# Optimization experiments

Hardware: AMD Instinct MI355X
Metric: run time of the kernel (lower is better)

## Reference

```python
import jax, jax.numpy as jnp
import numpy as np

NUM_POINTS = 4_000_000
RADIUS = 2.5
IMG = 1024


def setup_inputs() -> dict:
    key = jax.random.key(0)
    k1, k2, k3, k4 = jax.random.split(key, 4)
    # Uniform sampling inside a sphere, mirroring the torch __init__
    phi = jax.random.uniform(k1, (NUM_POINTS,)) * 2 * np.pi
    costheta = jax.random.uniform(k2, (NUM_POINTS,)) * 2 - 1
    u = jax.random.uniform(k3, (NUM_POINTS,))
    theta = jnp.arccos(costheta)
    r = RADIUS * u ** (1.0 / 3.0)
    x = r * jnp.sin(theta) * jnp.cos(phi)
    y = r * jnp.sin(theta) * jnp.sin(phi)
    z = r * jnp.cos(theta)
    positions = jnp.stack([x, y, z], axis=-1).astype(jnp.float32)  # [N,3]
    colors = jax.random.uniform(k4, (NUM_POINTS, 3), dtype=jnp.float32)
    # Camera at origin looking down +z, points translated to z in [2.5, 7.5]
    camera_pose = jnp.eye(4, dtype=jnp.float32).at[2, 3].set(5.0)
    intrinsics = jnp.array([[800.0, 0.0, 512.0],
                            [0.0, 800.0, 512.0],
                            [0.0, 0.0, 1.0]], dtype=jnp.float32)
    return {"positions": positions, "colors": colors,
            "camera_pose": camera_pose, "intrinsics": intrinsics,
            "H": IMG, "W": IMG}


def reference(positions, colors, camera_pose, intrinsics, H, W):
    # points_cam = (R @ P^T)^T + t^T
    R = camera_pose[:3, :3]
    t = camera_pose[:3, 3]
    pc = positions @ R.T + t  # [N,3]
    x, y, z = pc[:, 0], pc[:, 1], pc[:, 2]
    fx, fy = intrinsics[0, 0], intrinsics[1, 1]
    cx, cy = intrinsics[0, 2], intrinsics[1, 2]
    u = fx * x / z + cx
    v = fy * y / z + cy
    # int() truncation toward zero, matching the torch loop
    xi = u.astype(jnp.int32)
    yi = v.astype(jnp.int32)
    valid = (xi >= 0) & (xi < W) & (yi >= 0) & (yi < H)
    n = positions.shape[0]
    pix = jnp.where(valid, yi * W + xi, H * W)  # invalid -> sentinel segment
    winner = jax.ops.segment_max(jnp.arange(n, dtype=jnp.int32), pix,
                                 num_segments=H * W + 1)[: H * W]
    has = winner >= 0  # empty segments get iinfo(int32).min
    img_flat = jnp.where(has[:, None],
                         colors[jnp.clip(winner, 0, n - 1)],
                         jnp.float32(0.0))  # [H*W, 3]
    img = img_flat.reshape(H, W, 3).transpose(2, 0, 1)[None]  # [1,3,H,W]
    return jnp.clip(img, 0.0, 1.0)
```

## Files before the change

### kernel.cpp

```cpp
#include <hip/hip_runtime.h>


#define NB      512
#define TB      512
#define NT      1024
#define PPB_MAX 7936
#define IMGW    1024
#define IMGHW   (1024 * 1024)

__host__ __device__ __forceinline__ unsigned align8(unsigned x) {
    return (x + 7u) & ~7u;
}

__global__ void __launch_bounds__(TB)
binsort_kernel(const float* __restrict__ pos,
               const float* __restrict__ pose,
               const float* __restrict__ intr,
               unsigned* __restrict__ bins,
               unsigned* __restrict__ histG,
               int n, int ppb, int region) {
    __shared__ unsigned stash[PPB_MAX];
    __shared__ unsigned h[NT];
    __shared__ unsigned base_[NT];
    __shared__ unsigned cur[NT];
    __shared__ unsigned sc[TB];

    int tid = threadIdx.x;
    for (int t = tid; t < NT; t += TB) h[t] = 0;
    __syncthreads();

    float r00 = pose[0], r01 = pose[1], r02 = pose[2],  t0 = pose[3];
    float r10 = pose[4], r11 = pose[5], r12 = pose[6],  t1 = pose[7];
    float r20 = pose[8], r21 = pose[9], r22 = pose[10], t2 = pose[11];
    float fx = intr[0], cx = intr[2];
    float fy = intr[4], cy = intr[5];

    int start = blockIdx.x * ppb;
    int cnt = min(start + ppb, n) - start;
    if (cnt < 0) cnt = 0;

    for (int j = tid; j < cnt; j += TB) {
        int i = start + j;
        float px = pos[3 * i + 0];
        float py = pos[3 * i + 1];
        float pz = pos[3 * i + 2];
        float x = r00 * px + r01 * py + r02 * pz + t0;
        float y = r10 * px + r11 * py + r12 * pz + t1;
        float z = r20 * px + r21 * py + r22 * pz + t2;
        float u = fx * x / z + cx;
        float v = fy * y / z + cy;
        int xi = (int)u;
        int yi = (int)v;
        unsigned pv = 0xFFFFFFFFu;
        if (xi >= 0 && xi < IMGW && yi >= 0 && yi < IMGW) {
            pv = ((unsigned)yi << 10) | (unsigned)xi;
            int t = ((yi >> 5) << 5) + (xi >> 5);
            atomicAdd(&h[t], 1u);
        }
        stash[j] = pv;
    }
    __syncthreads();

    unsigned a0 = align8(h[2 * tid]);
    unsigned a1 = align8(h[2 * tid + 1]);
    unsigned v = a0 + a1;
    sc[tid] = v;
    __syncthreads();
    for (int off = 1; off < TB; off <<= 1) {
        unsigned add = (tid >= off) ? sc[tid - off] : 0u;
        __syncthreads();
        v += add;
        sc[tid] = v;
        __syncthreads();
    }
    base_[2 * tid]     = v - a0 - a1;
    base_[2 * tid + 1] = v - a1;
    __syncthreads();

    for (int t = tid; t < NT; t += TB) {
        cur[t] = base_[t];
        histG[(size_t)t * NB + blockIdx.x] = (base_[t] << 16) | h[t];
    }
    __syncthreads();

    unsigned* myRegion = bins + (size_t)blockIdx.x * (size_t)region;
    for (int j = tid; j < cnt; j += TB) {
        unsigned pv = stash[j];
        if (pv == 0xFFFFFFFFu) continue;
        unsigned xi = pv & 1023u, yi = pv >> 10;
        unsigned t  = ((yi >> 5) << 5) + (xi >> 5);
        unsigned lp = ((yi & 31u) << 5) + (xi & 31u);
        unsigned slot = atomicAdd(&cur[t], 1u);
        myRegion[slot] = (lp << 22) | (unsigned)(start + j);
    }
}

__global__ void __launch_bounds__(TB)
paint_kernel(const unsigned* __restrict__ bins,
             const unsigned* __restrict__ histG,
             const float* __restrict__ colors,
             float* __restrict__ out,
             int region) {
    __shared__ unsigned win[NT];
    int t = blockIdx.x;
    int tid = threadIdx.x;
    for (int l = tid; l < NT; l += TB) win[l] = 0;
    __syncthreads();

    unsigned pk = histG[(size_t)t * NB + tid];
    unsigned sbase = pk >> 16, cnt = pk & 0xFFFFu;
    const unsigned* seg = bins + (size_t)tid * (size_t)region + sbase;
    for (unsigned k = 0; k < cnt; ++k) {
        unsigned e = seg[k];
        atomicMax(&win[e >> 22], (e & 0x3FFFFFu) + 1u);
    }
    __syncthreads();

    int tx = (t & 31) << 5, ty = (t >> 5) << 5;
    for (int l = tid; l < NT; l += TB) {
        unsigned w = win[l];
        float r = 0.0f, g = 0.0f, bl = 0.0f;
        if (w) {
            unsigned wi = w - 1u;
            r  = fminf(fmaxf(colors[3 * wi + 0], 0.0f), 1.0f);
            g  = fminf(fmaxf(colors[3 * wi + 1], 0.0f), 1.0f);
            bl = fminf(fmaxf(colors[3 * wi + 2], 0.0f), 1.0f);
        }
        int x = tx + (l & 31), y = ty + (l >> 5);
        int p = y * IMGW + x;
        out[p] = r;
        out[IMGHW + p] = g;
        out[2 * IMGHW + p] = bl;
    }
}


__global__ void proj_simple(const float* __restrict__ pos,
                            const float* __restrict__ pose,
                            const float* __restrict__ intr,
                            const int* __restrict__ Hp,
                            const int* __restrict__ Wp,
                            int* __restrict__ winner, int n) {
    int i = blockIdx.x * blockDim.x + threadIdx.x;
    if (i >= n) return;
    float px = pos[3 * i], py = pos[3 * i + 1], pz = pos[3 * i + 2];
    float x = pose[0] * px + pose[1] * py + pose[2]  * pz + pose[3];
    float y = pose[4] * px + pose[5] * py + pose[6]  * pz + pose[7];
    float z = pose[8] * px + pose[9] * py + pose[10] * pz + pose[11];
    float u = intr[0] * x / z + intr[2];
    float v = intr[4] * y / z + intr[5];
    int xi = (int)u, yi = (int)v;
    int W = *Wp, H = *Hp;
    if (xi >= 0 && xi < W && yi >= 0 && yi < H) atomicMax(&winner[yi * W + xi], i);
}

__global__ void paint_simple(const int* __restrict__ winner,
                             const float* __restrict__ colors,
                             float* __restrict__ out, int HW) {
    int p = blockIdx.x * blockDim.x + threadIdx.x;
    if (p >= HW) return;
    int w = winner[p];
    float r = 0.0f, g = 0.0f, b = 0.0f;
    if (w >= 0) {
        r = fminf(fmaxf(colors[3 * w + 0], 0.0f), 1.0f);
        g = fminf(fmaxf(colors[3 * w + 1], 0.0f), 1.0f);
        b = fminf(fmaxf(colors[3 * w + 2], 0.0f), 1.0f);
    }
    out[p] = r; out[HW + p] = g; out[2 * HW + p] = b;
}

extern "C" void kernel_launch(void* const* d_in, const int* in_sizes, int n_in,
                              void* d_out, int out_size, void* d_ws, size_t ws_size,
                              hipStream_t stream) {
    const float* positions = (const float*)d_in[0];
    const float* colors    = (const float*)d_in[1];
    const float* pose      = (const float*)d_in[2];
    const float* intr      = (const float*)d_in[3];
    const int*   Hp        = (const int*)d_in[4];
    const int*   Wp        = (const int*)d_in[5];
    float* out = (float*)d_out;

    int n  = in_sizes[0] / 3;
    int HW = out_size / 3;

    int ppb = (n + NB - 1) / NB;
    int region = (int)align8((unsigned)ppb) + 7 * NT;
    unsigned* bins  = (unsigned*)d_ws;
    unsigned* histG = bins + (size_t)NB * (size_t)region;
    size_t needFast = ((size_t)NB * region + (size_t)NT * NB) * sizeof(unsigned);

    bool fast = (HW == IMGHW) && (n >= 4096) && (ppb <= PPB_MAX) &&
                (n <= 4000000) && (ws_size >= needFast);

    if (fast) {
        binsort_kernel<<<NB, TB, 0, stream>>>(positions, pose, intr,
                                              bins, histG, n, ppb, region);
        paint_kernel<<<NT, TB, 0, stream>>>(bins, histG, colors, out, region);
        return;
    }

    int* winner = (int*)d_ws;
    const int block = 256;
    hipMemsetAsync(winner, 0xFF, (size_t)HW * sizeof(int), stream);
    int grid = (n + block - 1) / block;
    proj_simple<<<grid, block, 0, stream>>>(positions, pose, intr, Hp, Wp,
                                            winner, n);
    int grid2 = (HW + block - 1) / block;
    paint_simple<<<grid2, block, 0, stream>>>(winner, colors, out, HW);
}
```

Baseline: 63.72 us.

## Double binning blocks, vectorize position loads, drop per-tile segment padding

Doubles the number of binning blocks so each one handles about 3900 points, and gives each thread four points per step loaded as three float4 values. The stash write becomes a single uint4 store. Per-tile bin segments are no longer padded to multiples of 8, which shrinks each block's region to just its point count. In the paint kernel each thread now walks two source-block segments instead of one, which adds serial work per paint block in exchange for finer and less padded binning.

Measured after the change: 70.71 us. +11.0%, slower.

```diff
diff --git a/kernel.cpp b/kernel.cpp
--- a/kernel.cpp
+++ b/kernel.cpp
@@ -1,14 +1,14 @@
 #include <hip/hip_runtime.h>
 
 
-#define NB      512
+#define NB      1024
 #define TB      512
 #define NT      1024
-#define PPB_MAX 7936
+#define PPB_MAX 4096
 #define IMGW    1024
 #define IMGHW   (1024 * 1024)
 
-__host__ __device__ __forceinline__ unsigned align8(unsigned x) {
+__host__ __device__ __forceinline__ unsigned align8u(unsigned x) {
     return (x + 7u) & ~7u;
 }
 
@@ -39,31 +39,53 @@
     int cnt = min(start + ppb, n) - start;
     if (cnt < 0) cnt = 0;
 
-    for (int j = tid; j < cnt; j += TB) {
-        int i = start + j;
-        float px = pos[3 * i + 0];
-        float py = pos[3 * i + 1];
-        float pz = pos[3 * i + 2];
-        float x = r00 * px + r01 * py + r02 * pz + t0;
-        float y = r10 * px + r11 * py + r12 * pz + t1;
-        float z = r20 * px + r21 * py + r22 * pz + t2;
-        float u = fx * x / z + cx;
-        float v = fy * y / z + cy;
-        int xi = (int)u;
-        int yi = (int)v;
-        unsigned pv = 0xFFFFFFFFu;
-        if (xi >= 0 && xi < IMGW && yi >= 0 && yi < IMGW) {
-            pv = ((unsigned)yi << 10) | (unsigned)xi;
-            int t = ((yi >> 5) << 5) + (xi >> 5);
-            atomicAdd(&h[t], 1u);
-        }
-        stash[j] = pv;
-    }
-    __syncthreads();
-
-    unsigned a0 = align8(h[2 * tid]);
-    unsigned a1 = align8(h[2 * tid + 1]);
-    unsigned v = a0 + a1;
+    const float4* p4 = (const float4*)(pos + (size_t)3 * (size_t)start);
+    for (int j4 = tid * 4; j4 < cnt; j4 += TB * 4) {
+        int g = j4 >> 2;
+        float4 A = p4[3 * g + 0];
+        float4 B = p4[3 * g + 1];
+        float4 C = p4[3 * g + 2];
+        float xs0 = A.x, ys0 = A.y, zs0 = A.z;
+        float xs1 = A.w, ys1 = B.x, zs1 = B.y;
+        float xs2 = B.z, ys2 = B.w, zs2 = C.x;
+        float xs3 = C.y, ys3 = C.z, zs3 = C.w;
+
+        unsigned pv[4];
+        #define PROJ(K, PX, PY, PZ)                                          \
+        {                                                                    \
+            float x = r00 * PX + r01 * PY + r02 * PZ + t0;                   \
+            float y = r10 * PX + r11 * PY + r12 * PZ + t1;                   \
+            float z = r20 * PX + r21 * PY + r22 * PZ + t2;                   \
+            float u = fx * x / z + cx;                                       \
+            float v = fy * y / z + cy;                                       \
+            int xi = (int)u;                                                 \
+            int yi = (int)v;                                                 \
+            unsigned p = 0xFFFFFFFFu;                                        \
+            if ((j4 + K) < cnt && xi >= 0 && xi < IMGW && yi >= 0 &&         \
+                yi < IMGW) {                                                 \
+                p = ((unsigned)yi << 10) | (unsigned)xi;                     \
+                int tt = ((yi >> 5) << 5) + (xi >> 5);                       \
+                atomicAdd(&h[tt], 1u);                                       \
+            }                                                                \
+            pv[K] = p;                                                       \
+        }
+        PROJ(0, xs0, ys0, zs0)
+        PROJ(1, xs1, ys1, zs1)
+        PROJ(2, xs2, ys2, zs2)
+        PROJ(3, xs3, ys3, zs3)
+        #undef PROJ
+
+        if (j4 + 3 < cnt) {
+            *(uint4*)&stash[j4] = make_uint4(pv[0], pv[1], pv[2], pv[3]);
+        } else {
+            for (int k = 0; k < 4 && j4 + k < cnt; ++k) stash[j4 + k] = pv[k];
+        }
+    }
+    __syncthreads();
+
+    unsigned c0 = h[2 * tid];
+    unsigned c1 = h[2 * tid + 1];
+    unsigned v = c0 + c1;
     sc[tid] = v;
     __syncthreads();
     for (int off = 1; off < TB; off <<= 1) {
@@ -73,8 +95,8 @@
         sc[tid] = v;
         __syncthreads();
     }
-    base_[2 * tid]     = v - a0 - a1;
-    base_[2 * tid + 1] = v - a1;
+    base_[2 * tid]     = v - c0 - c1;
+    base_[2 * tid + 1] = v - c1;
     __syncthreads();
 
     for (int t = tid; t < NT; t += TB) {
@@ -107,12 +129,14 @@
     for (int l = tid; l < NT; l += TB) win[l] = 0;
     __syncthreads();
 
-    unsigned pk = histG[(size_t)t * NB + tid];
-    unsigned sbase = pk >> 16, cnt = pk & 0xFFFFu;
-    const unsigned* seg = bins + (size_t)tid * (size_t)region + sbase;
-    for (unsigned k = 0; k < cnt; ++k) {
-        unsigned e = seg[k];
-        atomicMax(&win[e >> 22], (e & 0x3FFFFFu) + 1u);
+    for (int b = tid; b < NB; b += TB) {
+        unsigned pk = histG[(size_t)t * NB + b];
+        unsigned sbase = pk >> 16, cnt = pk & 0xFFFFu;
+        const unsigned* seg = bins + (size_t)b * (size_t)region + sbase;
+        for (unsigned k = 0; k < cnt; ++k) {
+            unsigned e = seg[k];
+            atomicMax(&win[e >> 22], (e & 0x3FFFFFu) + 1u);
+        }
     }
     __syncthreads();
 
@@ -183,8 +207,8 @@
     int n  = in_sizes[0] / 3;
     int HW = out_size / 3;
 
-    int ppb = (n + NB - 1) / NB;
-    int region = (int)align8((unsigned)ppb) + 7 * NT;
+    int ppb = ((n + NB - 1) / NB + 3) & ~3;
+    int region = (int)align8u((unsigned)ppb);
     unsigned* bins  = (unsigned*)d_ws;
     unsigned* histG = bins + (size_t)NB * (size_t)region;
     size_t needFast = ((size_t)NB * region + (size_t)NT * NB) * sizeof(unsigned);
```
